# Kernel tuning notes

Measured on AMD Instinct MI355X. Metric: run time of the kernel, lower is better.

The kernel has to match this reference:

```python
import jax, jax.numpy as jnp
import numpy as np

B, N, D = 4, 10000, 64
C, E = 2, 160000  # adj channels, edges per (graph, channel)
EPS = 1e-10


def setup_inputs() -> dict:
    key = jax.random.key(0)
    k1, k2, k3 = jax.random.split(key, 3)
    inputs = jax.random.normal(k1, (B, N, D), dtype=jnp.float32)
    edge_idx = jax.random.randint(k2, (B, C, E, 2), 0, N, dtype=jnp.int32)
    weight_a = 0.1 * jax.random.normal(k3, (C, 2 * D, 1), dtype=jnp.float32)
    return {"inputs": inputs, "edge_idx": edge_idx, "weight_a": weight_a}


def _gat_channel(x, idx, wa):
    # x: [N, D], idx: [E, 2] (col 0 = scatter/dst node, col 1 = gather/src node), wa: [2D, 1]
    n = x.shape[0]
    a1 = x[idx[:, 1]]                      # [E, D]
    a2 = x[idx[:, 0]]                      # [E, D]
    score = jnp.concatenate([a1, a2], axis=1) @ wa   # [E, 1]
    e = jnp.exp(jax.nn.leaky_relu(score, negative_slope=0.2))  # [E, 1]
    denom = jax.ops.segment_sum(e, idx[:, 0], num_segments=n)  # [N, 1]  (ii @ e)
    denom_e = denom[idx[:, 1]]             # [E, 1]  (faithful to original: gather by idx[:,1])
    alpha = e / (denom_e + EPS)            # [E, 1]
    r = jax.ops.segment_sum(alpha * a1, idx[:, 0], num_segments=n)  # [N, D]
    return jax.nn.sigmoid(r)


def _gat_graph(x, idx_all, weight_a):
    # x: [N, D], idx_all: [C, E, 2], weight_a: [C, 2D, 1]
    per_ch = jax.vmap(_gat_channel, in_axes=(None, 0, 0))(x, idx_all, weight_a)  # [C, N, D]
    return per_ch.sum(axis=0)


def reference(inputs, edge_idx, weight_a):
    # inputs: [B, N, D], edge_idx: [B, C, E, 2], weight_a: [C, 2D, 1]
    return jax.vmap(_gat_graph, in_axes=(0, 0, None))(inputs, edge_idx, weight_a)
```

## Files before the change

kernel.cpp:

```cpp
#include <hip/hip_runtime.h>

#define B_ 4
#define N_ 10000
#define D_ 64
#define C_ 2
#define E_ 160000
#define BC_ (B_ * C_)
#define SH2_ 7
#define NB2_ 128
#define G2_ 79
#define CAPF_ 2560
#define NBLK_ 125
#define EPB_ 1280
#define YBLK_ (B_ * 40)
#define POISON_ 0xAAAAAAAAu
#define EPS_ 1e-10f

__global__ void gat_yb(const float* __restrict__ x, const float* __restrict__ wa,
                       float* __restrict__ y1, float* __restrict__ y0,
                       const int* __restrict__ eidx, int* __restrict__ gcount,
                       unsigned int* __restrict__ bpack) {
    int tid = threadIdx.x;
    if (blockIdx.x < YBLK_) {
        int b = blockIdx.x & 3;
        int n = (blockIdx.x >> 2) * 256 + tid;
        if (n >= N_) return;
        const float4* xr = (const float4*)(x + ((size_t)b * N_ + n) * D_);
        const float4* wp = (const float4*)wa;
        float a0 = 0.f, b0 = 0.f, a1 = 0.f, b1 = 0.f;
#pragma unroll
        for (int i = 0; i < D_ / 4; ++i) {
            float4 xv = xr[i];
            float4 u0 = wp[i], v0 = wp[i + 16];
            float4 u1 = wp[i + 32], v1 = wp[i + 48];
            a0 += xv.x * u0.x + xv.y * u0.y + xv.z * u0.z + xv.w * u0.w;
            b0 += xv.x * v0.x + xv.y * v0.y + xv.z * v0.z + xv.w * v0.w;
            a1 += xv.x * u1.x + xv.y * u1.y + xv.z * u1.z + xv.w * u1.w;
            b1 += xv.x * v1.x + xv.y * v1.y + xv.z * v1.z + xv.w * v1.w;
        }
        int bc0 = b * C_;
        y1[bc0 * N_ + n] = a0;
        y0[bc0 * N_ + n] = b0;
        y1[(bc0 + 1) * N_ + n] = a1;
        y0[(bc0 + 1) * N_ + n] = b1;
        return;
    }
    int bid = blockIdx.x - YBLK_;
    int bc  = bid & 7;
    int blk = bid >> 3;
    const int4* ep4 = (const int4*)((const int2*)eidx + (size_t)bc * E_ +
                                    (size_t)blk * EPB_);
    __shared__ int sd[128];
    __shared__ int excl[G2_], cur[G2_], gbase[G2_];
    __shared__ unsigned int stage[EPB_];
    if (tid < 128) sd[tid] = 0;
    __syncthreads();
    int ne = (tid < 128) ? 6 : 4;
    unsigned int pk[6];
    int gg[6];
    {
        int4 q = ep4[tid];
        gg[0] = q.x >> SH2_;
        pk[0] = ((unsigned int)gg[0] << 21) | ((unsigned int)(q.x & 127) << 14) | (unsigned int)q.y;
        gg[1] = q.z >> SH2_;
        pk[1] = ((unsigned int)gg[1] << 21) | ((unsigned int)(q.z & 127) << 14) | (unsigned int)q.w;
        q = ep4[tid + 256];
        gg[2] = q.x >> SH2_;
        pk[2] = ((unsigned int)gg[2] << 21) | ((unsigned int)(q.x & 127) << 14) | (unsigned int)q.y;
        gg[3] = q.z >> SH2_;
        pk[3] = ((unsigned int)gg[3] << 21) | ((unsigned int)(q.z & 127) << 14) | (unsigned int)q.w;
        if (tid < 128) {
            q = ep4[tid + 512];
            gg[4] = q.x >> SH2_;
            pk[4] = ((unsigned int)gg[4] << 21) | ((unsigned int)(q.x & 127) << 14) | (unsigned int)q.y;
            gg[5] = q.z >> SH2_;
            pk[5] = ((unsigned int)gg[5] << 21) | ((unsigned int)(q.z & 127) << 14) | (unsigned int)q.w;
        }
    }
    for (int k = 0; k < ne; ++k) atomicAdd(&sd[gg[k]], 1);
    __syncthreads();
    int cnt = (tid < 128) ? sd[tid] : 0;
    __syncthreads();
    if (tid < 64) {
        int v0 = sd[2 * tid], v1 = sd[2 * tid + 1];
        int s = v0 + v1;
#pragma unroll
        for (int off = 1; off < 64; off <<= 1) {
            int t = __shfl_up(s, off);
            if (tid >= off) s += t;
        }
        sd[2 * tid]     = s - v1;
        sd[2 * tid + 1] = s;
    }
    __syncthreads();
    if (tid < G2_) {
        int ex = sd[tid] - cnt;
        excl[tid]  = ex;
        cur[tid]   = ex;
        unsigned int ret = (unsigned int)atomicAdd(&gcount[bc * G2_ + tid], cnt);
        gbase[tid] = (int)(ret - POISON_);
    }
    __syncthreads();
    for (int k = 0; k < ne; ++k) {
        int slot = atomicAdd(&cur[gg[k]], 1);
        stage[slot] = pk[k];
    }
    __syncthreads();
#pragma unroll
    for (int k = 0; k < 5; ++k) {
        int idx = k * 256 + tid;
        unsigned int p = stage[idx];
        int g     = p >> 21;
        int local = idx - excl[g];
        bpack[((size_t)bc * G2_ + g) * CAPF_ + gbase[g] + local] =
            (((p >> 14) & 127u) << 16) | (p & 16383u);
    }
}

__global__ void gat_fine(const unsigned int* __restrict__ bpack,
                         const int* __restrict__ gcount,
                         const float* __restrict__ y1, const float* __restrict__ y0,
                         unsigned short* __restrict__ csr_i1,
                         int* __restrict__ rs_s, int* __restrict__ rs_e,
                         float2* __restrict__ yrd) {
    int bc = blockIdx.x & 7;
    int g  = blockIdx.x >> 3;
    int K  = (int)((unsigned int)gcount[bc * G2_ + g] - POISON_);
    int R  = (bc * G2_ + g) * CAPF_;
    const unsigned int* bp = bpack + R;
    const float* y1p = y1 + bc * N_;
    int tid = threadIdx.x;

    __shared__ int   cnt[NB2_], sd[NB2_], cur[NB2_];
    __shared__ float y0l[NB2_], den[NB2_];

    int node = g * NB2_ + tid;
    if (tid < NB2_) {
        cnt[tid] = 0;
        den[tid] = 0.f;
        y0l[tid] = (node < N_) ? y0[bc * N_ + node] : 0.f;
    }
    __syncthreads();

    for (int j = tid; j < K; j += 256) {
        unsigned int p = bp[j];
        int ln = p >> 16;
        int i1 = p & 0xffff;
        float sc = y1p[i1] + y0l[ln];
        float ev = __expf(sc > 0.f ? sc : 0.2f * sc);
        atomicAdd(&cnt[ln], 1);
        atomicAdd(&den[ln], ev);
    }
    __syncthreads();

    if (tid < 64) {
        int v0 = cnt[2 * tid], v1 = cnt[2 * tid + 1];
        int s = v0 + v1;
#pragma unroll
        for (int off = 1; off < 64; off <<= 1) {
            int t = __shfl_up(s, off);
            if (tid >= off) s += t;
        }
        sd[2 * tid]     = s - v1;
        sd[2 * tid + 1] = s;
    }
    __syncthreads();
    if (tid < NB2_) {
        int v  = cnt[tid];
        int ex = sd[tid] - v;
        cur[tid] = ex;
        if (node < N_) {
            rs_s[bc * N_ + node] = R + ex;
            rs_e[bc * N_ + node] = R + ex + v;
            yrd[bc * N_ + node]  = make_float2(y1p[node], 1.f / (den[tid] + EPS_));
        }
    }
    __syncthreads();

    for (int j = tid; j < K; j += 256) {
        unsigned int p = bp[j];
        int slot = atomicAdd(&cur[p >> 16], 1);
        csr_i1[R + slot] = (unsigned short)(p & 0xffff);
    }
}

__global__ void gat_acc(const float* __restrict__ x, const int* __restrict__ rs_s,
                        const int* __restrict__ rs_e,
                        const unsigned short* __restrict__ csr_i1,
                        const float2* __restrict__ yrd, const float* __restrict__ y0,
                        float* __restrict__ out) {
    int lane = threadIdx.x & 63;
    int w    = threadIdx.x >> 6;
    int b    = blockIdx.x & 3;
    int gp   = blockIdx.x >> 2;
    int c    = w & 1;
    int n0   = gp * 8 + (w >> 1) * 4;
    int bc   = b * C_ + c;
    const float* xb = x + (size_t)b * N_ * D_ + lane;
    const float2* yrdp = yrd + bc * N_;
    int4   sv  = *(const int4*)(rs_s + bc * N_ + n0);
    int4   ev  = *(const int4*)(rs_e + bc * N_ + n0);
    float4 y04 = *(const float4*)(y0 + bc * N_ + n0);
    int s0 = sv.x;
    int e0 = ev.x, e1 = ev.y, e2 = ev.z, e3 = ev.w;
    __shared__ float2 meta[4][64];
    float acc0 = 0.f, acc1 = 0.f, acc2 = 0.f, acc3 = 0.f;

    int pa = 0; float2 pyr = make_float2(0.f, 0.f);
    {
        int idx = s0 + lane;
        if (idx < e3) { pa = csr_i1[idx]; pyr = yrdp[pa]; }
    }
    for (int base = s0; base < e3; base += 64) {
        int idx = base + lane;
        float wgt = 0.f;
        if (idx < e3) {
            float yn = idx < e0 ? y04.x : idx < e1 ? y04.y : idx < e2 ? y04.z : y04.w;
            float sc = pyr.x + yn;
            wgt = __expf(sc > 0.f ? sc : 0.2f * sc) * pyr.y;
        }
        meta[w][lane] = make_float2(__int_as_float(pa), wgt);
        int na = 0; float2 nyr = make_float2(0.f, 0.f);
        int nidx = base + 64 + lane;
        if (base + 64 < e3 && nidx < e3) { na = csr_i1[nidx]; nyr = yrdp[na]; }
        int hi = (base + 64 < e3) ? base + 64 : e3;
#define ACC_NODE(SK, EK, ACCK)                                                \
        {                                                                     \
            int lo = (SK > base) ? SK : base;                                 \
            int h  = (EK < hi) ? EK : hi;                                     \
            int j  = lo;                                                      \
            for (; j + 4 <= h; j += 4) {                                      \
                float2 m0 = meta[w][j - base];                                \
                float2 m1 = meta[w][j - base + 1];                            \
                float2 m2 = meta[w][j - base + 2];                            \
                float2 m3 = meta[w][j - base + 3];                            \
                float x0 = xb[__float_as_int(m0.x) * D_];                     \
                float x1 = xb[__float_as_int(m1.x) * D_];                     \
                float x2 = xb[__float_as_int(m2.x) * D_];                     \
                float x3 = xb[__float_as_int(m3.x) * D_];                     \
                ACCK += m0.y * x0;                                            \
                ACCK += m1.y * x1;                                            \
                ACCK += m2.y * x2;                                            \
                ACCK += m3.y * x3;                                            \
            }                                                                 \
            for (; j < h; ++j) {                                              \
                float2 mm = meta[w][j - base];                                \
                ACCK += mm.y * xb[__float_as_int(mm.x) * D_];                 \
            }                                                                 \
        }
        ACC_NODE(s0, e0, acc0)
        ACC_NODE(e0, e1, acc1)
        ACC_NODE(e1, e2, acc2)
        ACC_NODE(e2, e3, acc3)
#undef ACC_NODE
        pa = na; pyr = nyr;
    }
    float4 sg;
    sg.x = 1.f / (1.f + __expf(-acc0));
    sg.y = 1.f / (1.f + __expf(-acc1));
    sg.z = 1.f / (1.f + __expf(-acc2));
    sg.w = 1.f / (1.f + __expf(-acc3));
    __shared__ float sh[2][4][64];
    if (c == 1) {
        sh[w >> 1][0][lane] = sg.x;
        sh[w >> 1][1][lane] = sg.y;
        sh[w >> 1][2][lane] = sg.z;
        sh[w >> 1][3][lane] = sg.w;
    }
    __syncthreads();
    if (c == 0) {
        int h = w >> 1;
        out[((size_t)b * N_ + n0 + 0) * D_ + lane] = sg.x + sh[h][0][lane];
        out[((size_t)b * N_ + n0 + 1) * D_ + lane] = sg.y + sh[h][1][lane];
        out[((size_t)b * N_ + n0 + 2) * D_ + lane] = sg.z + sh[h][2][lane];
        out[((size_t)b * N_ + n0 + 3) * D_ + lane] = sg.w + sh[h][3][lane];
    }
}

extern "C" void kernel_launch(void* const* d_in, const int* in_sizes, int n_in,
                              void* d_out, int out_size, void* d_ws, size_t ws_size,
                              hipStream_t stream) {
    const float* x    = (const float*)d_in[0];
    const int*   eidx = (const int*)d_in[1];
    const float* wa   = (const float*)d_in[2];
    float* out = (float*)d_out;

    int*    gcount = (int*)d_ws;
    float*  y1     = (float*)d_ws + 2048;
    float*  y0     = y1 + BC_ * N_;
    float2* yrd    = (float2*)(y0 + BC_ * N_);
    int*    rs_s   = (int*)(yrd + BC_ * N_);
    int*    rs_e   = rs_s + BC_ * N_;
    unsigned int* bpack = (unsigned int*)(rs_e + BC_ * N_);
    unsigned short* csr_i1 = (unsigned short*)(bpack + (size_t)BC_ * G2_ * CAPF_);

    gat_yb  <<<YBLK_ + BC_ * NBLK_, 256, 0, stream>>>(x, wa, y1, y0, eidx, gcount, bpack);
    gat_fine<<<BC_ * G2_,           256, 0, stream>>>(bpack, gcount, y1, y0,
                                                      csr_i1, rs_s, rs_e, yrd);
    gat_acc <<<B_ * N_ / 8,         256, 0, stream>>>(x, rs_s, rs_e, csr_i1, yrd, y0, out);
}
```

Measured before the change: 124.6 us.

## Reuse atomic slot returns, stage CSR in LDS, and split edge gathers across half-waves

The bucketing kernel now keeps the return value of its counting atomic as each edge's local slot, which removes the second atomic pass. The fine kernel caches packed edges and their slots in LDS, sorts them into an LDS buffer, and writes the CSR out with coalesced 32-bit stores instead of scattered 16-bit stores. The accumulate kernel has each half-wave handle alternate edges, loading float2 per lane, then combines the halves with a cross-lane shuffle. This halves the serial gather chain per edge but adds LDS pressure in the fine kernel and leaves half the lanes idle on odd-tail edges.

```diff
diff --git a/kernel.cpp b/kernel.cpp
--- a/kernel.cpp
+++ b/kernel.cpp
@@ -51,13 +51,14 @@
     const int4* ep4 = (const int4*)((const int2*)eidx + (size_t)bc * E_ +
                                     (size_t)blk * EPB_);
     __shared__ int sd[128];
-    __shared__ int excl[G2_], cur[G2_], gbase[G2_];
+    __shared__ int excl[G2_], gbase[G2_];
     __shared__ unsigned int stage[EPB_];
     if (tid < 128) sd[tid] = 0;
     __syncthreads();
     int ne = (tid < 128) ? 6 : 4;
     unsigned int pk[6];
     int gg[6];
+    int slotk[6];
     {
         int4 q = ep4[tid];
         gg[0] = q.x >> SH2_;
@@ -77,7 +78,7 @@
             pk[5] = ((unsigned int)gg[5] << 21) | ((unsigned int)(q.z & 127) << 14) | (unsigned int)q.w;
         }
     }
-    for (int k = 0; k < ne; ++k) atomicAdd(&sd[gg[k]], 1);
+    for (int k = 0; k < ne; ++k) slotk[k] = atomicAdd(&sd[gg[k]], 1);
     __syncthreads();
     int cnt = (tid < 128) ? sd[tid] : 0;
     __syncthreads();
@@ -96,15 +97,11 @@
     if (tid < G2_) {
         int ex = sd[tid] - cnt;
         excl[tid]  = ex;
-        cur[tid]   = ex;
         unsigned int ret = (unsigned int)atomicAdd(&gcount[bc * G2_ + tid], cnt);
         gbase[tid] = (int)(ret - POISON_);
     }
     __syncthreads();
-    for (int k = 0; k < ne; ++k) {
-        int slot = atomicAdd(&cur[gg[k]], 1);
-        stage[slot] = pk[k];
-    }
+    for (int k = 0; k < ne; ++k) stage[excl[gg[k]] + slotk[k]] = pk[k];
     __syncthreads();
 #pragma unroll
     for (int k = 0; k < 5; ++k) {
@@ -131,8 +128,11 @@
     const float* y1p = y1 + bc * N_;
     int tid = threadIdx.x;
 
-    __shared__ int   cnt[NB2_], sd[NB2_], cur[NB2_];
+    __shared__ int   cnt[NB2_], sd[NB2_];
     __shared__ float y0l[NB2_], den[NB2_];
+    __shared__ unsigned int spk[CAPF_];
+    __shared__ __align__(4) unsigned short sslot[CAPF_];
+    __shared__ __align__(4) unsigned short ssort[CAPF_];
 
     int node = g * NB2_ + tid;
     if (tid < NB2_) {
@@ -148,8 +148,10 @@
         int i1 = p & 0xffff;
         float sc = y1p[i1] + y0l[ln];
         float ev = __expf(sc > 0.f ? sc : 0.2f * sc);
-        atomicAdd(&cnt[ln], 1);
+        int slot = atomicAdd(&cnt[ln], 1);
         atomicAdd(&den[ln], ev);
+        spk[j]   = p;
+        sslot[j] = (unsigned short)slot;
     }
     __syncthreads();
 
@@ -168,7 +170,7 @@
     if (tid < NB2_) {
         int v  = cnt[tid];
         int ex = sd[tid] - v;
-        cur[tid] = ex;
+        cnt[tid] = ex;
         if (node < N_) {
             rs_s[bc * N_ + node] = R + ex;
             rs_e[bc * N_ + node] = R + ex + v;
@@ -178,9 +180,16 @@
     __syncthreads();
 
     for (int j = tid; j < K; j += 256) {
-        unsigned int p = bp[j];
-        int slot = atomicAdd(&cur[p >> 16], 1);
-        csr_i1[R + slot] = (unsigned short)(p & 0xffff);
+        unsigned int p = spk[j];
+        int pos = cnt[p >> 16] + (int)sslot[j];
+        ssort[pos] = (unsigned short)(p & 0xffff);
+    }
+    __syncthreads();
+    {
+        const unsigned int* s32 = (const unsigned int*)ssort;
+        unsigned int* c32 = (unsigned int*)(csr_i1 + R);
+        int Kw = (K + 1) >> 1;
+        for (int j = tid; j < Kw; j += 256) c32[j] = s32[j];
     }
 }
 
@@ -196,15 +205,18 @@
     int c    = w & 1;
     int n0   = gp * 8 + (w >> 1) * 4;
     int bc   = b * C_ + c;
-    const float* xb = x + (size_t)b * N_ * D_ + lane;
+    int half = lane >> 5;
+    int col  = lane & 31;
+    const float2* xb2 = (const float2*)(x + (size_t)b * N_ * D_) + col;
     const float2* yrdp = yrd + bc * N_;
     int4   sv  = *(const int4*)(rs_s + bc * N_ + n0);
-    int4   ev  = *(const int4*)(rs_e + bc * N_ + n0);
+    int4   evv = *(const int4*)(rs_e + bc * N_ + n0);
     float4 y04 = *(const float4*)(y0 + bc * N_ + n0);
     int s0 = sv.x;
-    int e0 = ev.x, e1 = ev.y, e2 = ev.z, e3 = ev.w;
+    int e0 = evv.x, e1 = evv.y, e2 = evv.z, e3 = evv.w;
     __shared__ float2 meta[4][64];
-    float acc0 = 0.f, acc1 = 0.f, acc2 = 0.f, acc3 = 0.f;
+    float2 acc0 = make_float2(0.f, 0.f), acc1 = make_float2(0.f, 0.f);
+    float2 acc2 = make_float2(0.f, 0.f), acc3 = make_float2(0.f, 0.f);
 
     int pa = 0; float2 pyr = make_float2(0.f, 0.f);
     {
@@ -234,18 +246,28 @@
                 float2 m1 = meta[w][j - base + 1];                            \
                 float2 m2 = meta[w][j - base + 2];                            \
                 float2 m3 = meta[w][j - base + 3];                            \
-                float x0 = xb[__float_as_int(m0.x) * D_];                     \
-                float x1 = xb[__float_as_int(m1.x) * D_];                     \
-                float x2 = xb[__float_as_int(m2.x) * D_];                     \
-                float x3 = xb[__float_as_int(m3.x) * D_];                     \
-                ACCK += m0.y * x0;                                            \
-                ACCK += m1.y * x1;                                            \
-                ACCK += m2.y * x2;                                            \
-                ACCK += m3.y * x3;                                            \
+                float2 ma = half ? m1 : m0;                                   \
+                float2 mb = half ? m3 : m2;                                   \
+                float2 xa = xb2[__float_as_int(ma.x) * 32];                   \
+                float2 xc = xb2[__float_as_int(mb.x) * 32];                   \
+                ACCK.x += ma.y * xa.x;                                        \
+                ACCK.y += ma.y * xa.y;                                        \
+                ACCK.x += mb.y * xc.x;                                        \
+                ACCK.y += mb.y * xc.y;                                        \
             }                                                                 \
-            for (; j < h; ++j) {                                              \
+            for (; j + 2 <= h; j += 2) {                                      \
+                float2 m0 = meta[w][j - base];                                \
+                float2 m1 = meta[w][j - base + 1];                            \
+                float2 ma = half ? m1 : m0;                                   \
+                float2 xa = xb2[__float_as_int(ma.x) * 32];                   \
+                ACCK.x += ma.y * xa.x;                                        \
+                ACCK.y += ma.y * xa.y;                                        \
+            }                                                                 \
+            if (j < h && !half) {                                             \
                 float2 mm = meta[w][j - base];                                \
-                ACCK += mm.y * xb[__float_as_int(mm.x) * D_];                 \
+                float2 xa = xb2[__float_as_int(mm.x) * 32];                   \
+                ACCK.x += mm.y * xa.x;                                        \
+                ACCK.y += mm.y * xa.y;                                        \
             }                                                                 \
         }
         ACC_NODE(s0, e0, acc0)
@@ -255,25 +277,34 @@
 #undef ACC_NODE
         pa = na; pyr = nyr;
     }
-    float4 sg;
-    sg.x = 1.f / (1.f + __expf(-acc0));
-    sg.y = 1.f / (1.f + __expf(-acc1));
-    sg.z = 1.f / (1.f + __expf(-acc2));
-    sg.w = 1.f / (1.f + __expf(-acc3));
-    __shared__ float sh[2][4][64];
-    if (c == 1) {
-        sh[w >> 1][0][lane] = sg.x;
-        sh[w >> 1][1][lane] = sg.y;
-        sh[w >> 1][2][lane] = sg.z;
-        sh[w >> 1][3][lane] = sg.w;
-    }
-    __syncthreads();
-    if (c == 0) {
-        int h = w >> 1;
-        out[((size_t)b * N_ + n0 + 0) * D_ + lane] = sg.x + sh[h][0][lane];
-        out[((size_t)b * N_ + n0 + 1) * D_ + lane] = sg.y + sh[h][1][lane];
-        out[((size_t)b * N_ + n0 + 2) * D_ + lane] = sg.z + sh[h][2][lane];
-        out[((size_t)b * N_ + n0 + 3) * D_ + lane] = sg.w + sh[h][3][lane];
+    acc0.x += __shfl_xor(acc0.x, 32); acc0.y += __shfl_xor(acc0.y, 32);
+    acc1.x += __shfl_xor(acc1.x, 32); acc1.y += __shfl_xor(acc1.y, 32);
+    acc2.x += __shfl_xor(acc2.x, 32); acc2.y += __shfl_xor(acc2.y, 32);
+    acc3.x += __shfl_xor(acc3.x, 32); acc3.y += __shfl_xor(acc3.y, 32);
+    float2 sg0, sg1, sg2, sg3;
+    sg0.x = 1.f / (1.f + __expf(-acc0.x)); sg0.y = 1.f / (1.f + __expf(-acc0.y));
+    sg1.x = 1.f / (1.f + __expf(-acc1.x)); sg1.y = 1.f / (1.f + __expf(-acc1.y));
+    sg2.x = 1.f / (1.f + __expf(-acc2.x)); sg2.y = 1.f / (1.f + __expf(-acc2.y));
+    sg3.x = 1.f / (1.f + __expf(-acc3.x)); sg3.y = 1.f / (1.f + __expf(-acc3.y));
+    __shared__ float2 sh2[2][4][32];
+    if (c == 1 && half == 0) {
+        int hq = w >> 1;
+        sh2[hq][0][col] = sg0;
+        sh2[hq][1][col] = sg1;
+        sh2[hq][2][col] = sg2;
+        sh2[hq][3][col] = sg3;
+    }
+    __syncthreads();
+    if (c == 0 && half == 0) {
+        int hq = w >> 1;
+        float2 o0 = sh2[hq][0][col]; o0.x += sg0.x; o0.y += sg0.y;
+        float2 o1 = sh2[hq][1][col]; o1.x += sg1.x; o1.y += sg1.y;
+        float2 o2 = sh2[hq][2][col]; o2.x += sg2.x; o2.y += sg2.y;
+        float2 o3 = sh2[hq][3][col]; o3.x += sg3.x; o3.y += sg3.y;
+        *((float2*)(out + ((size_t)b * N_ + n0 + 0) * D_) + col) = o0;
+        *((float2*)(out + ((size_t)b * N_ + n0 + 1) * D_) + col) = o1;
+        *((float2*)(out + ((size_t)b * N_ + n0 + 2) * D_) + col) = o2;
+        *((float2*)(out + ((size_t)b * N_ + n0 + 3) * D_) + col) = o3;
     }
 }
 
```

Result: slower. 128.1 us, median of 3 (+2.8%).
